# Kernel optimization log

Measured on AMD Instinct MI355X. Metric: run time of the kernel, lower is better.

Reference implementation:

```python
import jax, jax.numpy as jnp
import numpy as np

BITS = 4
GROUPSIZE = 128
MAXQ = 2 ** BITS - 1
PACK = 32 // BITS  # values packed per int32


def setup_inputs() -> dict:
    key = jax.random.key(0)
    k1, k2, k3, k4 = jax.random.split(key, 4)
    infeatures, outfeatures = 4096, 11008
    G = infeatures // GROUPSIZE  # 32 quantization groups
    x = jax.random.normal(k1, (16, 1, infeatures), dtype=jnp.float32)
    qweight = jax.random.randint(k2, (infeatures // PACK, outfeatures), 0, 2147483647, dtype=jnp.int32)
    scales = jax.random.uniform(k3, (G, outfeatures), dtype=jnp.float32)
    qzeros = jax.random.randint(k4, (G, outfeatures // PACK), 0, 2147483647, dtype=jnp.int32)
    return {"x": x, "qweight": qweight, "scales": scales, "qzeros": qzeros}


def _dequant(qweight, scales, qzeros):
    # shift amounts 0,4,8,...,28
    wf = jnp.arange(0, 32, BITS, dtype=jnp.int32)
    # unpack zero-points: [G, out/PACK, PACK] -> [G, 1, out]
    zeros = jnp.bitwise_and(jnp.right_shift(qzeros[:, :, None], wf[None, None, :]), MAXQ)
    zeros = zeros.reshape(zeros.shape[0], 1, -1).astype(scales.dtype)
    # unpack weights: [in/PACK, PACK, out] -> [G, GROUPSIZE, out]
    w = jnp.bitwise_and(jnp.right_shift(qweight[:, None, :], wf[None, :, None]), MAXQ)
    w = w.reshape(-1, GROUPSIZE, w.shape[-1]).astype(scales.dtype)
    sc = scales[:, None, :]  # [G, 1, out]
    weight = sc * w - sc * zeros  # per-group dequant
    return weight.reshape(-1, weight.shape[-1])  # [in, out]


def reference(x, qweight, scales, qzeros):
    W = _dequant(qweight, scales, qzeros)
    return jnp.matmul(x, W)  # [B, S, out]
```

## Files before the change

kernel.cpp:

```cpp
#include <hip/hip_runtime.h>


#define M_DIM 16
#define K_DIM 4096
#define N_DIM 11008
#define GS 128
#define KSPLIT 4
#define KC (K_DIM / KSPLIT)
#define GPC (KC / GS)
#define BLOCKN 64
#define NTHREADS 256

typedef __attribute__((ext_vector_type(8))) short short8;
typedef __attribute__((ext_vector_type(4))) float f32x4;

__device__ __forceinline__ float bfl(unsigned w) {
    union { unsigned u; float f; } c; c.u = w << 16; return c.f;
}
__device__ __forceinline__ float bfh(unsigned w) {
    union { unsigned u; float f; } c; c.u = w & 0xFFFF0000u; return c.f;
}

__global__ __launch_bounds__(NTHREADS) void qlin_fused(
    const float* __restrict__ x,
    const int*   __restrict__ qweight,
    const float* __restrict__ scales,
    const int*   __restrict__ qzeros,
    float*       __restrict__ out)
{
    __shared__ __align__(16) unsigned short xs[M_DIM * KC];
    __shared__ __align__(16) float Xl[GPC * 16];

    const int tid  = threadIdx.x;
    const int lane = tid & 63, wave = tid >> 6;
    const int lmod = lane & 15, lhi = lane >> 4;
    const int n    = blockIdx.x * BLOCKN + wave * 16 + lmod;
    const int swzA = (lmod & 7) << 4;
    const int zsh  = (n & 7) * 4;

    const int ky0 = blockIdx.y * KC;
    const int G0 = ky0 / GS, rowbase = ky0 >> 3;

#pragma unroll
    for (int i = 0; i < (M_DIM * KC / 8) / NTHREADS; ++i) {
        const int idx = i * NTHREADS + tid;
        const int m  = idx >> 7;
        const int cc = idx & 127;
        const float4* xp =
            (const float4*)(x + (size_t)m * K_DIM + ky0 + cc * 8);
        const float4 v0 = xp[0], v1 = xp[1];
        union { short8 s; unsigned u[4]; } pk;
        asm("v_cvt_pk_bf16_f32 %0, %1, %2" : "=v"(pk.u[0]) : "v"(v0.x), "v"(v1.x));
        asm("v_cvt_pk_bf16_f32 %0, %1, %2" : "=v"(pk.u[1]) : "v"(v0.y), "v"(v1.y));
        asm("v_cvt_pk_bf16_f32 %0, %1, %2" : "=v"(pk.u[2]) : "v"(v0.z), "v"(v1.z));
        asm("v_cvt_pk_bf16_f32 %0, %1, %2" : "=v"(pk.u[3]) : "v"(v0.w), "v"(v1.w));
        const int byte = ((m * KC + cc * 8) * 2) ^ ((m & 7) << 4);
        *(short8*)((char*)xs + byte) = pk.s;
    }
    __syncthreads();

#pragma unroll
    for (int gg = wave; gg < GPC; gg += 4) {
        float xv = 0.f;
#pragma unroll
        for (int q = 0; q < 4; ++q) {
            const int byte =
                ((lmod * KC + gg * GS + lhi * 32 + q * 8) * 2) ^ swzA;
            union { short8 s; unsigned u[4]; } a;
            a.s = *(const short8*)((const char*)xs + byte);
#pragma unroll
            for (int p = 0; p < 4; ++p) xv += bfl(a.u[p]) + bfh(a.u[p]);
        }
        xv += __shfl_xor(xv, 16, 64);
        xv += __shfl_xor(xv, 32, 64);
        if (lane < 16) Xl[gg * 16 + lane] = xv;
    }
    __syncthreads();

    f32x4 outacc = {0.f, 0.f, 0.f, 0.f};
#pragma unroll
    for (int g = 0; g < GPC; ++g) {
        const float s = scales[(size_t)(G0 + g) * N_DIM + n];
        const unsigned zq =
            (unsigned)qzeros[(size_t)(G0 + g) * (N_DIM / 8) + (n >> 3)];
        f32x4 acc = {0.f, 0.f, 0.f, 0.f};
#pragma unroll
        for (int t = 0; t < 4; ++t) {
            const unsigned q = (unsigned)
                qweight[(size_t)(rowbase + g * 16 + t * 4 + lhi) * N_DIM + n];
            union { short8 v; unsigned u[4]; } b;
            b.u[0] = ( q        & 0x000F000Fu) | 0x43804380u;
            b.u[1] = ((q >> 4)  & 0x000F000Fu) | 0x43804380u;
            b.u[2] = ((q >> 8)  & 0x000F000Fu) | 0x43804380u;
            b.u[3] = ((q >> 12) & 0x000F000Fu) | 0x43804380u;
            const int byte =
                ((lmod * KC + g * GS + t * 32 + lhi * 8) * 2) ^ swzA;
            const short8 a = *(const short8*)((const char*)xs + byte);
            acc = __builtin_amdgcn_mfma_f32_16x16x32_bf16(a, b.v, acc, 0, 0, 0);
        }
        const f32x4 x4 = *(const f32x4*)&Xl[g * 16 + lhi * 4];
        const float z  = (float)((zq >> zsh) & 15u);
        const float s2 = 0.5f * s;
        const float zc = -s * (128.0f + z);
#pragma unroll
        for (int r = 0; r < 4; ++r)
            outacc[r] = fmaf(s2, acc[r], fmaf(zc, x4[r], outacc[r]));
    }

#pragma unroll
    for (int r = 0; r < 4; ++r)
        atomicAdd(&out[(size_t)(lhi * 4 + r) * N_DIM + n], outacc[r]);
}

extern "C" void kernel_launch(void* const* d_in, const int* in_sizes, int n_in,
                              void* d_out, int out_size, void* d_ws, size_t ws_size,
                              hipStream_t stream) {
    const float* x       = (const float*)d_in[0];
    const int*   qweight = (const int*)d_in[1];
    const float* scales  = (const float*)d_in[2];
    const int*   qzeros  = (const int*)d_in[3];
    float*       out     = (float*)d_out;

    hipMemsetAsync(out, 0, (size_t)out_size * sizeof(float), stream);
    dim3 grid(N_DIM / BLOCKN, KSPLIT);
    qlin_fused<<<grid, NTHREADS, 0, stream>>>(x, qweight, scales, qzeros, out);
}
```

Baseline: 18.07 us.

## Split into prep, MFMA, and reduce kernels with pre-laid-out bf16 activations

Moves the bf16 conversion of x and the per-group row sums into a separate prep kernel. That kernel writes activations already in MFMA fragment order to workspace, so the main kernel loads A fragments straight from global memory and needs no LDS or barriers. The K split grows from 4 to 8. Atomics and the memset are replaced by per-split partial outputs that a third kernel sums. In exchange it adds two kernel launches and about 5.6 MB of partial-result traffic to workspace.

```diff
diff --git a/kernel.cpp b/kernel.cpp
--- a/kernel.cpp
+++ b/kernel.cpp
@@ -5,9 +5,9 @@
 #define K_DIM 4096
 #define N_DIM 11008
 #define GS 128
-#define KSPLIT 4
-#define KC (K_DIM / KSPLIT)
-#define GPC (KC / GS)
+#define NG (K_DIM / GS)
+#define KSPLIT 8
+#define GPB 4
 #define BLOCKN 64
 #define NTHREADS 256
 
@@ -21,84 +21,80 @@
     union { unsigned u; float f; } c; c.u = w & 0xFFFF0000u; return c.f;
 }
 
-__global__ __launch_bounds__(NTHREADS) void qlin_fused(
+__global__ __launch_bounds__(256) void qlin_prep(
     const float* __restrict__ x,
+    unsigned short* __restrict__ xbf,
+    float* __restrict__ Xtab)
+{
+    const int g = blockIdx.x;
+    const int t = threadIdx.x;
+    const int m = t >> 4;
+    const int c = t & 15;
+    const float* xp = x + (size_t)m * K_DIM + g * GS + c * 8;
+
+    float v[8];
+#pragma unroll
+    for (int j = 0; j < 8; ++j) v[j] = xp[j];
+
+    union { short8 s; unsigned u[4]; } pk;
+    asm("v_cvt_pk_bf16_f32 %0, %1, %2" : "=v"(pk.u[0]) : "v"(v[0]), "v"(v[4]));
+    asm("v_cvt_pk_bf16_f32 %0, %1, %2" : "=v"(pk.u[1]) : "v"(v[1]), "v"(v[5]));
+    asm("v_cvt_pk_bf16_f32 %0, %1, %2" : "=v"(pk.u[2]) : "v"(v[2]), "v"(v[6]));
+    asm("v_cvt_pk_bf16_f32 %0, %1, %2" : "=v"(pk.u[3]) : "v"(v[3]), "v"(v[7]));
+
+    const int T    = g * 4 + (c >> 2);
+    const int lane = (c & 3) * 16 + m;
+    *(short8*)(xbf + (size_t)T * 512 + lane * 8) = pk.s;
+
+    float s = 0.f;
+#pragma unroll
+    for (int p = 0; p < 4; ++p) s += bfl(pk.u[p]) + bfh(pk.u[p]);
+    s += __shfl_xor(s, 1, 16);
+    s += __shfl_xor(s, 2, 16);
+    s += __shfl_xor(s, 4, 16);
+    s += __shfl_xor(s, 8, 16);
+    if (c == 0) Xtab[g * 16 + m] = s;
+}
+
+__global__ __launch_bounds__(NTHREADS) void qlin_mfma(
     const int*   __restrict__ qweight,
     const float* __restrict__ scales,
     const int*   __restrict__ qzeros,
-    float*       __restrict__ out)
+    const unsigned short* __restrict__ xbf,
+    const float* __restrict__ Xtab,
+    float*       __restrict__ part)
 {
-    __shared__ __align__(16) unsigned short xs[M_DIM * KC];
-    __shared__ __align__(16) float Xl[GPC * 16];
-
     const int tid  = threadIdx.x;
     const int lane = tid & 63, wave = tid >> 6;
     const int lmod = lane & 15, lhi = lane >> 4;
     const int n    = blockIdx.x * BLOCKN + wave * 16 + lmod;
-    const int swzA = (lmod & 7) << 4;
     const int zsh  = (n & 7) * 4;
+    const int G0   = blockIdx.y * GPB;
 
-    const int ky0 = blockIdx.y * KC;
-    const int G0 = ky0 / GS, rowbase = ky0 >> 3;
+    f32x4 outacc = {0.f, 0.f, 0.f, 0.f};
 
 #pragma unroll
-    for (int i = 0; i < (M_DIM * KC / 8) / NTHREADS; ++i) {
-        const int idx = i * NTHREADS + tid;
-        const int m  = idx >> 7;
-        const int cc = idx & 127;
-        const float4* xp =
-            (const float4*)(x + (size_t)m * K_DIM + ky0 + cc * 8);
-        const float4 v0 = xp[0], v1 = xp[1];
-        union { short8 s; unsigned u[4]; } pk;
-        asm("v_cvt_pk_bf16_f32 %0, %1, %2" : "=v"(pk.u[0]) : "v"(v0.x), "v"(v1.x));
-        asm("v_cvt_pk_bf16_f32 %0, %1, %2" : "=v"(pk.u[1]) : "v"(v0.y), "v"(v1.y));
-        asm("v_cvt_pk_bf16_f32 %0, %1, %2" : "=v"(pk.u[2]) : "v"(v0.z), "v"(v1.z));
-        asm("v_cvt_pk_bf16_f32 %0, %1, %2" : "=v"(pk.u[3]) : "v"(v0.w), "v"(v1.w));
-        const int byte = ((m * KC + cc * 8) * 2) ^ ((m & 7) << 4);
-        *(short8*)((char*)xs + byte) = pk.s;
-    }
-    __syncthreads();
+    for (int g = 0; g < GPB; ++g) {
+        const int G = G0 + g;
+        const float s = scales[(size_t)G * N_DIM + n];
+        const unsigned zq =
+            (unsigned)qzeros[(size_t)G * (N_DIM / 8) + (n >> 3)];
 
-#pragma unroll
-    for (int gg = wave; gg < GPC; gg += 4) {
-        float xv = 0.f;
-#pragma unroll
-        for (int q = 0; q < 4; ++q) {
-            const int byte =
-                ((lmod * KC + gg * GS + lhi * 32 + q * 8) * 2) ^ swzA;
-            union { short8 s; unsigned u[4]; } a;
-            a.s = *(const short8*)((const char*)xs + byte);
-#pragma unroll
-            for (int p = 0; p < 4; ++p) xv += bfl(a.u[p]) + bfh(a.u[p]);
-        }
-        xv += __shfl_xor(xv, 16, 64);
-        xv += __shfl_xor(xv, 32, 64);
-        if (lane < 16) Xl[gg * 16 + lane] = xv;
-    }
-    __syncthreads();
-
-    f32x4 outacc = {0.f, 0.f, 0.f, 0.f};
-#pragma unroll
-    for (int g = 0; g < GPC; ++g) {
-        const float s = scales[(size_t)(G0 + g) * N_DIM + n];
-        const unsigned zq =
-            (unsigned)qzeros[(size_t)(G0 + g) * (N_DIM / 8) + (n >> 3)];
         f32x4 acc = {0.f, 0.f, 0.f, 0.f};
 #pragma unroll
         for (int t = 0; t < 4; ++t) {
-            const unsigned q = (unsigned)
-                qweight[(size_t)(rowbase + g * 16 + t * 4 + lhi) * N_DIM + n];
+            const int T = G * 4 + t;
+            const short8 a = *(const short8*)(xbf + (size_t)T * 512 + lane * 8);
+            const unsigned q =
+                (unsigned)qweight[(size_t)(T * 4 + lhi) * N_DIM + n];
             union { short8 v; unsigned u[4]; } b;
             b.u[0] = ( q        & 0x000F000Fu) | 0x43804380u;
             b.u[1] = ((q >> 4)  & 0x000F000Fu) | 0x43804380u;
             b.u[2] = ((q >> 8)  & 0x000F000Fu) | 0x43804380u;
             b.u[3] = ((q >> 12) & 0x000F000Fu) | 0x43804380u;
-            const int byte =
-                ((lmod * KC + g * GS + t * 32 + lhi * 8) * 2) ^ swzA;
-            const short8 a = *(const short8*)((const char*)xs + byte);
             acc = __builtin_amdgcn_mfma_f32_16x16x32_bf16(a, b.v, acc, 0, 0, 0);
         }
-        const f32x4 x4 = *(const f32x4*)&Xl[g * 16 + lhi * 4];
+        const f32x4 x4 = *(const f32x4*)(Xtab + G * 16 + lhi * 4);
         const float z  = (float)((zq >> zsh) & 15u);
         const float s2 = 0.5f * s;
         const float zc = -s * (128.0f + z);
@@ -109,7 +105,20 @@
 
 #pragma unroll
     for (int r = 0; r < 4; ++r)
-        atomicAdd(&out[(size_t)(lhi * 4 + r) * N_DIM + n], outacc[r]);
+        part[(size_t)(blockIdx.y * M_DIM + lhi * 4 + r) * N_DIM + n] = outacc[r];
+}
+
+__global__ __launch_bounds__(256) void qlin_reduce(
+    const float* __restrict__ part, float* __restrict__ out)
+{
+    const int i = blockIdx.x * 256 + threadIdx.x;
+    if (i < M_DIM * N_DIM) {
+        float s = 0.f;
+#pragma unroll
+        for (int c = 0; c < KSPLIT; ++c)
+            s += part[(size_t)c * M_DIM * N_DIM + i];
+        out[i] = s;
+    }
 }
 
 extern "C" void kernel_launch(void* const* d_in, const int* in_sizes, int n_in,
@@ -121,7 +130,16 @@
     const int*   qzeros  = (const int*)d_in[3];
     float*       out     = (float*)d_out;
 
-    hipMemsetAsync(out, 0, (size_t)out_size * sizeof(float), stream);
+    const size_t xbf_bytes  = (size_t)128 * 512 * sizeof(unsigned short);
+    const size_t xtab_bytes = (size_t)NG * 16 * sizeof(float);
+    unsigned short* xbf  = (unsigned short*)d_ws;
+    float*          Xtab = (float*)((char*)d_ws + xbf_bytes);
+    float*          part = (float*)((char*)d_ws + xbf_bytes +
+                                    ((xtab_bytes + 255) & ~(size_t)255));
+
+    qlin_prep<<<NG, 256, 0, stream>>>(x, xbf, Xtab);
     dim3 grid(N_DIM / BLOCKN, KSPLIT);
-    qlin_fused<<<grid, NTHREADS, 0, stream>>>(x, qweight, scales, qzeros, out);
+    qlin_mfma<<<grid, NTHREADS, 0, stream>>>(qweight, scales, qzeros,
+                                             xbf, Xtab, part);
+    qlin_reduce<<<(M_DIM * N_DIM + 255) / 256, 256, 0, stream>>>(part, out);
 }
```

New measurement: 22.14 us. 1.22x slower.

## Split K across waves within one block, reduce in LDS, drop memset and atomics

Applied to the files above, without the earlier changes.

Each block now covers 16 output columns over the full K range, with 8 waves each taking 4 quantization groups. Partial sums are reduced through shared memory and written directly, so the output memset and global atomics go away. x is loaded and converted to bf16 straight from global memory into MFMA operands instead of being staged in LDS. Block indices are remapped to spread the column tiles. In exchange, every block rereads all of x from global/L2, and each wave writes to and reads from its own Xl entries with no barrier in between.

```diff
diff --git a/kernel.cpp b/kernel.cpp
--- a/kernel.cpp
+++ b/kernel.cpp
@@ -5,11 +5,11 @@
 #define K_DIM 4096
 #define N_DIM 11008
 #define GS 128
-#define KSPLIT 4
-#define KC (K_DIM / KSPLIT)
-#define GPC (KC / GS)
-#define BLOCKN 64
-#define NTHREADS 256
+#define NG (K_DIM / GS)
+#define WAVES 8
+#define GPW (NG / WAVES)
+#define NTHREADS 512
+#define NBLK (N_DIM / 16)
 
 typedef __attribute__((ext_vector_type(8))) short short8;
 typedef __attribute__((ext_vector_type(4))) float f32x4;
@@ -21,84 +21,63 @@
     union { unsigned u; float f; } c; c.u = w & 0xFFFF0000u; return c.f;
 }
 
-__global__ __launch_bounds__(NTHREADS) void qlin_fused(
+__global__ __launch_bounds__(NTHREADS) void qlin_one(
     const float* __restrict__ x,
     const int*   __restrict__ qweight,
     const float* __restrict__ scales,
     const int*   __restrict__ qzeros,
     float*       __restrict__ out)
 {
-    __shared__ __align__(16) unsigned short xs[M_DIM * KC];
-    __shared__ __align__(16) float Xl[GPC * 16];
+    __shared__ __align__(16) float Xl[NG * 16];
+    __shared__ __align__(16) f32x4 red[WAVES * 64];
 
     const int tid  = threadIdx.x;
     const int lane = tid & 63, wave = tid >> 6;
     const int lmod = lane & 15, lhi = lane >> 4;
-    const int n    = blockIdx.x * BLOCKN + wave * 16 + lmod;
-    const int swzA = (lmod & 7) << 4;
+    const int nb   = (blockIdx.x & 7) * (NBLK / 8) + (blockIdx.x >> 3);
+    const int n    = nb * 16 + lmod;
     const int zsh  = (n & 7) * 4;
+    const float* xrow = x + (size_t)lmod * K_DIM;
 
-    const int ky0 = blockIdx.y * KC;
-    const int G0 = ky0 / GS, rowbase = ky0 >> 3;
+    f32x4 outacc = {0.f, 0.f, 0.f, 0.f};
 
 #pragma unroll
-    for (int i = 0; i < (M_DIM * KC / 8) / NTHREADS; ++i) {
-        const int idx = i * NTHREADS + tid;
-        const int m  = idx >> 7;
-        const int cc = idx & 127;
-        const float4* xp =
-            (const float4*)(x + (size_t)m * K_DIM + ky0 + cc * 8);
-        const float4 v0 = xp[0], v1 = xp[1];
-        union { short8 s; unsigned u[4]; } pk;
-        asm("v_cvt_pk_bf16_f32 %0, %1, %2" : "=v"(pk.u[0]) : "v"(v0.x), "v"(v1.x));
-        asm("v_cvt_pk_bf16_f32 %0, %1, %2" : "=v"(pk.u[1]) : "v"(v0.y), "v"(v1.y));
-        asm("v_cvt_pk_bf16_f32 %0, %1, %2" : "=v"(pk.u[2]) : "v"(v0.z), "v"(v1.z));
-        asm("v_cvt_pk_bf16_f32 %0, %1, %2" : "=v"(pk.u[3]) : "v"(v0.w), "v"(v1.w));
-        const int byte = ((m * KC + cc * 8) * 2) ^ ((m & 7) << 4);
-        *(short8*)((char*)xs + byte) = pk.s;
-    }
-    __syncthreads();
+    for (int g = 0; g < GPW; ++g) {
+        const int G = wave * GPW + g;
+        const float s = scales[(size_t)G * N_DIM + n];
+        const unsigned zq =
+            (unsigned)qzeros[(size_t)G * (N_DIM / 8) + (n >> 3)];
 
-#pragma unroll
-    for (int gg = wave; gg < GPC; gg += 4) {
-        float xv = 0.f;
-#pragma unroll
-        for (int q = 0; q < 4; ++q) {
-            const int byte =
-                ((lmod * KC + gg * GS + lhi * 32 + q * 8) * 2) ^ swzA;
-            union { short8 s; unsigned u[4]; } a;
-            a.s = *(const short8*)((const char*)xs + byte);
-#pragma unroll
-            for (int p = 0; p < 4; ++p) xv += bfl(a.u[p]) + bfh(a.u[p]);
-        }
-        xv += __shfl_xor(xv, 16, 64);
-        xv += __shfl_xor(xv, 32, 64);
-        if (lane < 16) Xl[gg * 16 + lane] = xv;
-    }
-    __syncthreads();
-
-    f32x4 outacc = {0.f, 0.f, 0.f, 0.f};
-#pragma unroll
-    for (int g = 0; g < GPC; ++g) {
-        const float s = scales[(size_t)(G0 + g) * N_DIM + n];
-        const unsigned zq =
-            (unsigned)qzeros[(size_t)(G0 + g) * (N_DIM / 8) + (n >> 3)];
         f32x4 acc = {0.f, 0.f, 0.f, 0.f};
+        float xs = 0.f;
 #pragma unroll
         for (int t = 0; t < 4; ++t) {
-            const unsigned q = (unsigned)
-                qweight[(size_t)(rowbase + g * 16 + t * 4 + lhi) * N_DIM + n];
+            const int T = G * 4 + t;
+            const float4* xp = (const float4*)(xrow + T * 32 + lhi * 8);
+            const float4 v0 = xp[0], v1 = xp[1];
+            union { short8 sv; unsigned u[4]; } pk;
+            asm("v_cvt_pk_bf16_f32 %0, %1, %2" : "=v"(pk.u[0]) : "v"(v0.x), "v"(v1.x));
+            asm("v_cvt_pk_bf16_f32 %0, %1, %2" : "=v"(pk.u[1]) : "v"(v0.y), "v"(v1.y));
+            asm("v_cvt_pk_bf16_f32 %0, %1, %2" : "=v"(pk.u[2]) : "v"(v0.z), "v"(v1.z));
+            asm("v_cvt_pk_bf16_f32 %0, %1, %2" : "=v"(pk.u[3]) : "v"(v0.w), "v"(v1.w));
+
+            const unsigned q =
+                (unsigned)qweight[(size_t)(T * 4 + lhi) * N_DIM + n];
             union { short8 v; unsigned u[4]; } b;
             b.u[0] = ( q        & 0x000F000Fu) | 0x43804380u;
             b.u[1] = ((q >> 4)  & 0x000F000Fu) | 0x43804380u;
             b.u[2] = ((q >> 8)  & 0x000F000Fu) | 0x43804380u;
             b.u[3] = ((q >> 12) & 0x000F000Fu) | 0x43804380u;
-            const int byte =
-                ((lmod * KC + g * GS + t * 32 + lhi * 8) * 2) ^ swzA;
-            const short8 a = *(const short8*)((const char*)xs + byte);
-            acc = __builtin_amdgcn_mfma_f32_16x16x32_bf16(a, b.v, acc, 0, 0, 0);
+            acc = __builtin_amdgcn_mfma_f32_16x16x32_bf16(pk.sv, b.v, acc, 0, 0, 0);
+
+#pragma unroll
+            for (int p = 0; p < 4; ++p) xs += bfl(pk.u[p]) + bfh(pk.u[p]);
         }
-        const f32x4 x4 = *(const f32x4*)&Xl[g * 16 + lhi * 4];
+        xs += __shfl_xor(xs, 16, 64);
+        xs += __shfl_xor(xs, 32, 64);
+        if (lane < 16) Xl[G * 16 + lane] = xs;
+        const f32x4 x4 = *(const f32x4*)&Xl[G * 16 + lhi * 4];
+
         const float z  = (float)((zq >> zsh) & 15u);
         const float s2 = 0.5f * s;
         const float zc = -s * (128.0f + z);
@@ -107,9 +86,20 @@
             outacc[r] = fmaf(s2, acc[r], fmaf(zc, x4[r], outacc[r]));
     }
 
+    red[wave * 64 + lane] = outacc;
+    __syncthreads();
+    if (wave == 0) {
+        f32x4 sum = red[lane];
 #pragma unroll
-    for (int r = 0; r < 4; ++r)
-        atomicAdd(&out[(size_t)(lhi * 4 + r) * N_DIM + n], outacc[r]);
+        for (int w = 1; w < WAVES; ++w) {
+            const f32x4 rv = red[w * 64 + lane];
+#pragma unroll
+            for (int r = 0; r < 4; ++r) sum[r] += rv[r];
+        }
+#pragma unroll
+        for (int r = 0; r < 4; ++r)
+            out[(size_t)(lhi * 4 + r) * N_DIM + n] = sum[r];
+    }
 }
 
 extern "C" void kernel_launch(void* const* d_in, const int* in_sizes, int n_in,
@@ -121,7 +111,5 @@
     const int*   qzeros  = (const int*)d_in[3];
     float*       out     = (float*)d_out;
 
-    hipMemsetAsync(out, 0, (size_t)out_size * sizeof(float), stream);
-    dim3 grid(N_DIM / BLOCKN, KSPLIT);
-    qlin_fused<<<grid, NTHREADS, 0, stream>>>(x, qweight, scales, qzeros, out);
+    qlin_one<<<NBLK, NTHREADS, 0, stream>>>(x, qweight, scales, qzeros, out);
 }
```

Result: slower. 29.13 us (+61.2%).
